# Kernel tuning notes

Measured on AMD Instinct MI355X. Metric: run time of the kernel, lower is better.

The kernel has to match this reference:

```python
import jax, jax.numpy as jnp
import numpy as np

B, S, D = 64, 512, 1024


def setup_inputs() -> dict:
    key = jax.random.key(0)
    k_h, k_w = jax.random.split(key)
    last_hidden_state = jax.random.normal(k_h, (B, S, D), dtype=jnp.float32)
    # word_ids: sorted, contiguous subword->word indices per row (tokenizer word_ids).
    inc = jax.random.bernoulli(k_w, 0.5, (B, S)).astype(jnp.int32)
    inc = inc.at[:, 0].set(0)  # first token starts word 0
    word_ids = jnp.cumsum(inc, axis=1)  # [B, S], max ~ S/2 words
    return {"last_hidden_state": last_hidden_state, "word_ids": word_ids}


def reference(last_hidden_state, word_ids):
    # Faithful, vectorized version of merge_subword_representation:
    # out[i, w] = mean of last_hidden_state[i, t] over t with word_ids[i, t] == w,
    # for w in [0, tot_words_i); remaining positions keep original values.
    b, s, d = last_hidden_state.shape
    seg_sum = jax.vmap(
        lambda h, w: jax.ops.segment_sum(h, w, num_segments=s)
    )(last_hidden_state, word_ids)                                  # [B, S, D]
    cnt = jax.vmap(
        lambda w: jax.ops.segment_sum(jnp.ones((s,), last_hidden_state.dtype), w, num_segments=s)
    )(word_ids)                                                     # [B, S]
    means = seg_sum / jnp.maximum(cnt, 1.0)[..., None]              # safe: valid segments have cnt>=1
    tot_words = jnp.max(word_ids, axis=1) + 1                       # [B]
    pos = jnp.arange(s)
    write_mask = pos[None, :] < tot_words[:, None]                  # [B, S]
    return jnp.where(write_mask[..., None], means, last_hidden_state)
```

## Files before the change

kernel.cpp:

```cpp
#include <hip/hip_runtime.h>

#define BS 64
#define SS 512
#define DD 1024

__global__ __launch_bounds__(256) void merge_subword_kernel(
    const float* __restrict__ h,
    const int*   __restrict__ wid,
    float*       __restrict__ out)
{
    const int w = blockIdx.x;
    const int b = blockIdx.y;

    const int* row = wid + b * SS;

    __shared__ int s_lo, s_hi, s_tot;
    if (threadIdx.x == 0) {
        int tot = row[SS - 1] + 1;
        s_tot = tot;
        if (w < tot) {
            int lo = 0, hi = SS;
            while (lo < hi) {
                int m = (lo + hi) >> 1;
                if (row[m] < w) lo = m + 1; else hi = m;
            }
            s_lo = lo;
            int lo2 = lo, hi2 = SS;
            while (lo2 < hi2) {
                int m = (lo2 + hi2) >> 1;
                if (row[m] <= w) lo2 = m + 1; else hi2 = m;
            }
            s_hi = lo2;
        }
    }
    __syncthreads();

    const int tid = threadIdx.x;
    float4* dst = (float4*)(out + ((size_t)b * SS + w) * DD);

    if (w >= s_tot) {
        const float4* src = (const float4*)(h + ((size_t)b * SS + w) * DD);
        dst[tid] = src[tid];
    } else {
        const int lo = s_lo, hi = s_hi;
        const float inv = 1.0f / (float)(hi - lo);
        float4 acc = make_float4(0.f, 0.f, 0.f, 0.f);
        const float4* base = (const float4*)(h + ((size_t)b * SS + lo) * DD);
        const int nvec = DD / 4;
        for (int t = 0; t < hi - lo; ++t) {
            float4 v = base[(size_t)t * nvec + tid];
            acc.x += v.x; acc.y += v.y; acc.z += v.z; acc.w += v.w;
        }
        acc.x *= inv; acc.y *= inv; acc.z *= inv; acc.w *= inv;
        dst[tid] = acc;
    }
}

extern "C" void kernel_launch(void* const* d_in, const int* in_sizes, int n_in,
                              void* d_out, int out_size, void* d_ws, size_t ws_size,
                              hipStream_t stream) {
    (void)in_sizes; (void)n_in; (void)out_size; (void)d_ws; (void)ws_size;
    const float* h   = (const float*)d_in[0];
    const int*   wid = (const int*)d_in[1];
    float*       out = (float*)d_out;

    dim3 grid(SS, BS);
    dim3 block(256);
    merge_subword_kernel<<<grid, block, 0, stream>>>(h, wid, out);
}
```

Before: 56.63 us.

## Process eight words per block with shared-memory word ids and nontemporal stores

Each block now handles eight consecutive output rows instead of one, so the grid shrinks eightfold. The block stages the whole word_ids row in shared memory, and eight threads run the binary searches in parallel against it instead of a single thread reading global memory. Output writes use nontemporal stores to avoid polluting the cache. The trade-off is less parallelism per block and serialized row loops, which reduces memory-level parallelism per wave.

After: 58.10 us. 1.03x slower.

```diff
diff --git a/kernel.cpp b/kernel.cpp
--- a/kernel.cpp
+++ b/kernel.cpp
@@ -3,56 +3,59 @@
 #define BS 64
 #define SS 512
 #define DD 1024
+#define WPB 8
+#define NVEC (DD / 4)
+
+typedef float f4 __attribute__((ext_vector_type(4)));
 
 __global__ __launch_bounds__(256) void merge_subword_kernel(
     const float* __restrict__ h,
     const int*   __restrict__ wid,
     float*       __restrict__ out)
 {
-    const int w = blockIdx.x;
-    const int b = blockIdx.y;
+    const int chunk = blockIdx.x;
+    const int b     = blockIdx.y;
+    const int w0    = chunk * WPB;
+
+    __shared__ int s_wid[SS];
+    __shared__ int s_lo[WPB], s_hi[WPB];
 
     const int* row = wid + b * SS;
+    for (int i = threadIdx.x; i < SS; i += 256) s_wid[i] = row[i];
+    __syncthreads();
 
-    __shared__ int s_lo, s_hi, s_tot;
-    if (threadIdx.x == 0) {
-        int tot = row[SS - 1] + 1;
-        s_tot = tot;
-        if (w < tot) {
-            int lo = 0, hi = SS;
-            while (lo < hi) {
-                int m = (lo + hi) >> 1;
-                if (row[m] < w) lo = m + 1; else hi = m;
-            }
-            s_lo = lo;
-            int lo2 = lo, hi2 = SS;
-            while (lo2 < hi2) {
-                int m = (lo2 + hi2) >> 1;
-                if (row[m] <= w) lo2 = m + 1; else hi2 = m;
-            }
-            s_hi = lo2;
-        }
+    if (threadIdx.x < WPB) {
+        const int w = w0 + (int)threadIdx.x;
+        int lo = 0, hi = SS;
+        while (lo < hi) { int m = (lo + hi) >> 1; if (s_wid[m] < w) lo = m + 1; else hi = m; }
+        s_lo[threadIdx.x] = lo;
+        int lo2 = lo, hi2 = SS;
+        while (lo2 < hi2) { int m = (lo2 + hi2) >> 1; if (s_wid[m] <= w) lo2 = m + 1; else hi2 = m; }
+        s_hi[threadIdx.x] = lo2;
     }
     __syncthreads();
 
+    const int tot = s_wid[SS - 1] + 1;
     const int tid = threadIdx.x;
-    float4* dst = (float4*)(out + ((size_t)b * SS + w) * DD);
 
-    if (w >= s_tot) {
-        const float4* src = (const float4*)(h + ((size_t)b * SS + w) * DD);
-        dst[tid] = src[tid];
-    } else {
-        const int lo = s_lo, hi = s_hi;
-        const float inv = 1.0f / (float)(hi - lo);
-        float4 acc = make_float4(0.f, 0.f, 0.f, 0.f);
-        const float4* base = (const float4*)(h + ((size_t)b * SS + lo) * DD);
-        const int nvec = DD / 4;
-        for (int t = 0; t < hi - lo; ++t) {
-            float4 v = base[(size_t)t * nvec + tid];
-            acc.x += v.x; acc.y += v.y; acc.z += v.z; acc.w += v.w;
+    #pragma unroll
+    for (int k = 0; k < WPB; ++k) {
+        const int w = w0 + k;
+        f4* dst = (f4*)(out + ((size_t)b * SS + w) * DD);
+        if (w >= tot) {
+            const f4* src = (const f4*)(h + ((size_t)b * SS + w) * DD);
+            __builtin_nontemporal_store(src[tid], dst + tid);
+        } else {
+            const int lo = s_lo[k], hi = s_hi[k];
+            const float inv = 1.0f / (float)(hi - lo);
+            f4 acc = (f4)(0.f);
+            const f4* base = (const f4*)(h + ((size_t)b * SS + lo) * DD);
+            for (int t = 0; t < hi - lo; ++t) {
+                acc += base[(size_t)t * NVEC + tid];
+            }
+            acc *= inv;
+            __builtin_nontemporal_store(acc, dst + tid);
         }
-        acc.x *= inv; acc.y *= inv; acc.z *= inv; acc.w *= inv;
-        dst[tid] = acc;
     }
 }
 
@@ -64,7 +67,7 @@
     const int*   wid = (const int*)d_in[1];
     float*       out = (float*)d_out;
 
-    dim3 grid(SS, BS);
+    dim3 grid(SS / WPB, BS);
     dim3 block(256);
     merge_subword_kernel<<<grid, block, 0, stream>>>(h, wid, out);
 }
```
